# Kernel optimization log

Hardware: AMD Instinct MI355X
Metric: run time of the kernel (lower is better)

The kernel has to match this reference:

```python
import jax, jax.numpy as jnp
import numpy as np
import math

SIZE = (60, 270, 480)           # full video T, H, W
CHANNELS = 14                   # sum of per-level grid channels 8+4+2
GRID_SIZES = [(60, 16, 16, 8), (30, 8, 8, 4), (15, 4, 4, 2)]
IDX_MAX = (60, 3, 5)            # patch grid -> patch_size (1, 90, 96)
PADDING = (0, 1, 1)
N_PATCH = 64
MANIP_LBASE = 2.0
MANIP_LEVELS = 8
INIT_SCALE = 1e-3


def setup_inputs() -> dict:
    key = jax.random.key(0)
    kt, kh, kw = jax.random.split(key, 3)
    idx = jnp.stack([
        jax.random.randint(kt, (N_PATCH,), 0, IDX_MAX[0]),
        jax.random.randint(kh, (N_PATCH,), 0, IDX_MAX[1]),
        jax.random.randint(kw, (N_PATCH,), 0, IDX_MAX[2]),
    ], axis=1).astype(jnp.int32)
    inp = {
        "idx": idx,
        "idx_max": jnp.asarray(IDX_MAX, dtype=jnp.int32),
        "padding": jnp.asarray(PADDING, dtype=jnp.int32),
    }
    for i, (T, H, W, C) in enumerate(GRID_SIZES):
        k = jax.random.fold_in(key, 10 + i)
        inp[f"grid{i}"] = jax.random.normal(k, (T * H * W, C), jnp.float32) * INIT_SCALE
    return inp


def _pixel_idx_1d(ix, size_d, nmax_d, pad_d):
    # ix: [N] patch index along one dim -> ([N, P+2*pad] clipped pixel idx, mask)
    p = size_d // nmax_d
    offs = jnp.arange(-pad_d, p + pad_d)
    raw = ix[:, None] * p + offs[None, :]
    mask = ((raw >= 0) & (raw < size_d)).astype(jnp.float32)
    return jnp.clip(raw, 0, size_d - 1), mask


def reference(idx, idx_max, padding, grid0, grid1, grid2):
    T, H, W = SIZE
    im = tuple(int(v) for v in np.asarray(idx_max))
    pad = tuple(int(v) for v in np.asarray(padding))
    patch = tuple(SIZE[d] // im[d] for d in range(3))
    ppad = tuple(patch[d] + 2 * pad[d] for d in range(3))

    # Multi-level grids -> trilinear upsample to full (T,H,W,C_i), concat on C.
    # jax.image.resize 'trilinear' uses half-pixel centers == torch align_corners=False.
    enc_splits = []
    for g, (Tg, Hg, Wg, Cg) in zip((grid0, grid1, grid2), GRID_SIZES):
        enc_splits.append(jax.image.resize(g.reshape(Tg, Hg, Wg, Cg), (T, H, W, Cg), method="trilinear"))
    enc = jnp.concatenate(enc_splits, axis=-1).reshape(T * H * W, CHANNELS)

    it, mt = _pixel_idx_1d(idx[:, 0], T, im[0], pad[0])
    ih, mh = _pixel_idx_1d(idx[:, 1], H, im[1], pad[1])
    iw, mw = _pixel_idx_1d(idx[:, 2], W, im[2], pad[2])

    flat = (it[:, :, None, None] * (H * W) + ih[:, None, :, None] * W + iw[:, None, None, :]).reshape(-1)
    mask = (mt[:, :, None, None] * mh[:, None, :, None] * mw[:, None, None, :]).reshape(-1, 1)

    t_embed = (mask * enc[flat]).reshape((idx.shape[0],) + ppad + (CHANNELS,))

    bases = (MANIP_LBASE ** jnp.arange(MANIP_LEVELS, dtype=jnp.float32)) * math.pi
    v = idx[:, 0].astype(jnp.float32)[:, None] * bases
    t_manip = jnp.concatenate([jnp.sin(v), jnp.cos(v)], axis=-1)  # [N, 2*levels]

    return t_embed, t_manip
```

## Files before the change

### kernel.cpp

```cpp
#include <hip/hip_runtime.h>
#include <math.h>


#define N_PATCH 64
#define PPAD_H 92
#define PPAD_W 98
#define CH 14
#define ROWS_PER_BLOCK 4
#define BLOCKS_PER_PATCH 23
#define ELEMS_PER_ROW (PPAD_W * CH)
#define ELEMS_PER_PATCH (PPAD_H * ELEMS_PER_ROW)
#define TOTAL_EMBED (N_PATCH * ELEMS_PER_PATCH)
#define TOTAL_MANIP (N_PATCH * 16)

#define RB_STRIDE 72
#define L1_OFF 48
#define L2_OFF 64
#define V_ENTRIES (ROWS_PER_BLOCK * 70)

__device__ __forceinline__ float lerpf(float a, float b, float f) {
    return a + f * (b - a);
}

__device__ __forceinline__ int wcell0(int rw0, float sw, int Wg) {
    float x = ((float)rw0 + 0.5f) * sw - 0.5f;
    int w0 = (int)floorf(x);
    return min(max(w0, 0), Wg - 1);
}

__global__ __launch_bounds__(256) void embed_kernel(
    const int* __restrict__ idx,
    const float* __restrict__ g0,
    const float* __restrict__ g1,
    const float* __restrict__ g2,
    float* __restrict__ out)
{
    __shared__ __align__(16) float s_V[ROWS_PER_BLOCK * RB_STRIDE];
    __shared__ float4 s_wl[3][PPAD_W];
    __shared__ __align__(16) float s_buf[4 * 64 * CH];

    const int tid = threadIdx.x;
    const int bx  = blockIdx.x;
    const int n   = blockIdx.y;
    const int it  = idx[3 * n + 0];
    const int ih  = idx[3 * n + 1];
    const int iw  = idx[3 * n + 2];
    const int rw0 = iw * 96 - 1;
    const int row0 = bx * ROWS_PER_BLOCK;

    const float sw0 = (float)((double)16 / 480.0);
    const float sw1 = (float)((double)8  / 480.0);
    const float sw2 = (float)((double)4  / 480.0);
    const float sh0 = (float)((double)16 / 270.0);
    const float sh1 = (float)((double)8  / 270.0);
    const float sh2 = (float)((double)4  / 270.0);

    if (bx == 0 && n == 0) {
        float* om = out + TOTAL_EMBED;
        for (int e = tid; e < TOTAL_MANIP; e += 256) {
            int nn = e >> 4;
            int j  = e & 15;
            int l  = j & 7;
            float base = (float)M_PI * (float)(1 << l);
            float v = (float)idx[3 * nn + 0] * base;
            double dv = (double)v;
            om[e] = (float)((j < 8) ? sin(dv) : cos(dv));
        }
    }

    const int C0_0 = wcell0(rw0, sw0, 16);
    const int C0_1 = wcell0(rw0, sw1, 8);
    const int C0_2 = wcell0(rw0, sw2, 4);
    for (int e = tid; e < V_ENTRIES; e += 256) {
        int row = e / 70;
        int off = e - 70 * row;
        int rh  = ih * 90 + row0 + row - 1;
        float mh = ((unsigned)rh < 270u) ? 1.0f : 0.0f;
        float v;
        if (off < L1_OFF) {
            int cell = off >> 3, chn = off & 7;
            float xh = ((float)rh + 0.5f) * sh0 - 0.5f;
            float ff = floorf(xh);
            float fh = xh - ff;
            int h0 = (int)ff;
            int h0c = min(max(h0, 0), 15), h1c = min(h0 + 1, 15);
            int cw = min(C0_0 + cell, 15);
            const float* base = g0 + (size_t)it * 2048;
            float a = base[(h0c * 16 + cw) * 8 + chn];
            float b = base[(h1c * 16 + cw) * 8 + chn];
            v = mh * lerpf(a, b, fh);
        } else if (off < L2_OFF) {
            int o = off - L1_OFF;
            int cell = o >> 2, chn = o & 3;
            float xh = ((float)rh + 0.5f) * sh1 - 0.5f;
            float ff = floorf(xh);
            float fh = xh - ff;
            int h0 = (int)ff;
            int h0c = min(max(h0, 0), 7), h1c = min(h0 + 1, 7);
            float xt = ((float)it + 0.5f) * 0.5f - 0.5f;
            float ftf = floorf(xt);
            float ft  = xt - ftf;
            int t0 = (int)ftf;
            int t0c = min(max(t0, 0), 29), t1c = min(t0 + 1, 29);
            int cw = min(C0_1 + cell, 7);
            float a00 = g1[((t0c * 8 + h0c) * 8 + cw) * 4 + chn];
            float a01 = g1[((t0c * 8 + h1c) * 8 + cw) * 4 + chn];
            float a10 = g1[((t1c * 8 + h0c) * 8 + cw) * 4 + chn];
            float a11 = g1[((t1c * 8 + h1c) * 8 + cw) * 4 + chn];
            v = mh * lerpf(lerpf(a00, a01, fh), lerpf(a10, a11, fh), ft);
        } else {
            int o = off - L2_OFF;
            int cell = o >> 1, chn = o & 1;
            float xh = ((float)rh + 0.5f) * sh2 - 0.5f;
            float ff = floorf(xh);
            float fh = xh - ff;
            int h0 = (int)ff;
            int h0c = min(max(h0, 0), 3), h1c = min(h0 + 1, 3);
            float xt = ((float)it + 0.5f) * 0.25f - 0.5f;
            float ftf = floorf(xt);
            float ft  = xt - ftf;
            int t0 = (int)ftf;
            int t0c = min(max(t0, 0), 14), t1c = min(t0 + 1, 14);
            int cw = min(C0_2 + cell, 3);
            float a00 = g2[((t0c * 4 + h0c) * 4 + cw) * 2 + chn];
            float a01 = g2[((t0c * 4 + h1c) * 4 + cw) * 2 + chn];
            float a10 = g2[((t1c * 4 + h0c) * 4 + cw) * 2 + chn];
            float a11 = g2[((t1c * 4 + h1c) * 4 + cw) * 2 + chn];
            v = mh * lerpf(lerpf(a00, a01, fh), lerpf(a10, a11, fh), ft);
        }
        s_V[row * RB_STRIDE + off] = v;
    }

    for (int i = tid; i < 3 * PPAD_W; i += 256) {
        int lvl = (i >= PPAD_W) + (i >= 2 * PPAD_W);
        int ww  = i - PPAD_W * lvl;
        int Wg  = (lvl == 0) ? 16 : ((lvl == 1) ? 8 : 4);
        int cs  = (lvl == 0) ? 8  : ((lvl == 1) ? 4 : 2);
        int bb  = (lvl == 0) ? 0  : ((lvl == 1) ? L1_OFF : L2_OFF);
        int C0  = (lvl == 0) ? C0_0 : ((lvl == 1) ? C0_1 : C0_2);
        float sw = (lvl == 0) ? sw0 : ((lvl == 1) ? sw1 : sw2);
        int rw = iw * 96 + ww - 1;
        float mask = ((unsigned)rw < 480u) ? 1.0f : 0.0f;
        float x  = ((float)rw + 0.5f) * sw - 0.5f;
        float ff = floorf(x);
        float f  = x - ff;
        int w0 = (int)ff;
        int wa = min(max(w0, 0), Wg - 1);
        int wb = min(w0 + 1, Wg - 1);
        s_wl[lvl][ww] = make_float4(__int_as_float(bb + (wa - C0) * cs),
                                    __int_as_float(bb + (wb - C0) * cs), f, mask);
    }

    __syncthreads();

    const int wv   = tid >> 6;
    const int lane = tid & 63;
    float* lbuf = s_buf + wv * (64 * CH);
    const float* V = s_V + wv * RB_STRIDE;
    float* orow = out + (size_t)n * ELEMS_PER_PATCH
                      + (size_t)(row0 + wv) * ELEMS_PER_ROW;

    #pragma unroll
    for (int s = 0; s < 2; ++s) {
        asm volatile("s_waitcnt lgkmcnt(0)" ::: "memory");
        __builtin_amdgcn_sched_barrier(0);
        int ww = s * 64 + lane;
        if (ww < PPAD_W) {
            float4 wl0 = s_wl[0][ww];
            float4 wl1 = s_wl[1][ww];
            float4 wl2 = s_wl[2][ww];
            int oA0 = __float_as_int(wl0.x), oB0 = __float_as_int(wl0.y);
            int oA1 = __float_as_int(wl1.x), oB1 = __float_as_int(wl1.y);
            int oA2 = __float_as_int(wl2.x), oB2 = __float_as_int(wl2.y);
            float fw0 = wl0.z, fw1 = wl1.z, fw2 = wl2.z, mw = wl0.w;

            float4 A0  = *(const float4*)(V + oA0);
            float4 A1  = *(const float4*)(V + oA0 + 4);
            float4 B0  = *(const float4*)(V + oB0);
            float4 B1  = *(const float4*)(V + oB0 + 4);
            float4 C1a = *(const float4*)(V + oA1);
            float4 C1b = *(const float4*)(V + oB1);
            float2 C2a = *(const float2*)(V + oA2);
            float2 C2b = *(const float2*)(V + oB2);

            float2* b = (float2*)(lbuf + lane * CH);
            b[0] = make_float2(mw * lerpf(A0.x, B0.x, fw0),
                               mw * lerpf(A0.y, B0.y, fw0));
            b[1] = make_float2(mw * lerpf(A0.z, B0.z, fw0),
                               mw * lerpf(A0.w, B0.w, fw0));
            b[2] = make_float2(mw * lerpf(A1.x, B1.x, fw0),
                               mw * lerpf(A1.y, B1.y, fw0));
            b[3] = make_float2(mw * lerpf(A1.z, B1.z, fw0),
                               mw * lerpf(A1.w, B1.w, fw0));
            b[4] = make_float2(mw * lerpf(C1a.x, C1b.x, fw1),
                               mw * lerpf(C1a.y, C1b.y, fw1));
            b[5] = make_float2(mw * lerpf(C1a.z, C1b.z, fw1),
                               mw * lerpf(C1a.w, C1b.w, fw1));
            b[6] = make_float2(mw * lerpf(C2a.x, C2b.x, fw2),
                               mw * lerpf(C2a.y, C2b.y, fw2));
        }
        __builtin_amdgcn_wave_barrier();
        asm volatile("s_waitcnt lgkmcnt(0)" ::: "memory");
        __builtin_amdgcn_sched_barrier(0);

        const int npx = (s == 0) ? 64 : (PPAD_W - 64);
        const int nf4 = npx * CH / 4;
        const float4* sb = (const float4*)lbuf;
        float4* gb = (float4*)(orow + s * 64 * CH);
        for (int j = lane; j < nf4; j += 64) gb[j] = sb[j];
        __builtin_amdgcn_wave_barrier();
    }
}

extern "C" void kernel_launch(void* const* d_in, const int* in_sizes, int n_in,
                              void* d_out, int out_size, void* d_ws, size_t ws_size,
                              hipStream_t stream) {
    const int*   idx = (const int*)  d_in[0];
    const float* g0  = (const float*)d_in[3];
    const float* g1  = (const float*)d_in[4];
    const float* g2  = (const float*)d_in[5];
    float* out = (float*)d_out;

    dim3 grid(BLOCKS_PER_PATCH, N_PATCH);
    embed_kernel<<<grid, 256, 0, stream>>>(idx, g0, g1, g2, out);
}
```

Baseline: 13.60 us.

## Split into table-precompute kernel and direct-store streaming kernel via workspace

Splits the fused kernel in two. The first kernel computes the per-row height/time-interpolated value table for all patches into a global workspace, plus the sin/cos manip output. The second kernel launches one block per output row, with each thread computing two channel pairs and writing one float4 straight to global memory, so there is no LDS staging. This removes the per-block shared-memory setup and the syncs, but adds a second launch and a round trip through global memory for the table.

```diff
diff --git a/kernel.cpp b/kernel.cpp
--- a/kernel.cpp
+++ b/kernel.cpp
@@ -6,17 +6,19 @@
 #define PPAD_H 92
 #define PPAD_W 98
 #define CH 14
-#define ROWS_PER_BLOCK 4
-#define BLOCKS_PER_PATCH 23
 #define ELEMS_PER_ROW (PPAD_W * CH)
+#define F4_PER_ROW (ELEMS_PER_ROW / 4)
 #define ELEMS_PER_PATCH (PPAD_H * ELEMS_PER_ROW)
+#define F4_PER_PATCH (ELEMS_PER_PATCH / 4)
 #define TOTAL_EMBED (N_PATCH * ELEMS_PER_PATCH)
 #define TOTAL_MANIP (N_PATCH * 16)
 
 #define RB_STRIDE 72
 #define L1_OFF 48
 #define L2_OFF 64
-#define V_ENTRIES (ROWS_PER_BLOCK * 70)
+#define ROWS_TOTAL (N_PATCH * PPAD_H)
+#define V_TOTAL (ROWS_TOTAL * 70)
+#define WS_PATCH (PPAD_H * RB_STRIDE)
 
 __device__ __forceinline__ float lerpf(float a, float b, float f) {
     return a + f * (b - a);
@@ -28,188 +30,163 @@
     return min(max(w0, 0), Wg - 1);
 }
 
-__global__ __launch_bounds__(256) void embed_kernel(
+#define SW0 ((float)((double)16 / 480.0))
+#define SW1 ((float)((double)8  / 480.0))
+#define SW2 ((float)((double)4  / 480.0))
+#define SH0 ((float)((double)16 / 270.0))
+#define SH1 ((float)((double)8  / 270.0))
+#define SH2 ((float)((double)4  / 270.0))
+
+__global__ __launch_bounds__(256) void vtab_kernel(
     const int* __restrict__ idx,
     const float* __restrict__ g0,
     const float* __restrict__ g1,
     const float* __restrict__ g2,
+    float* __restrict__ ws,
     float* __restrict__ out)
 {
-    __shared__ __align__(16) float s_V[ROWS_PER_BLOCK * RB_STRIDE];
-    __shared__ float4 s_wl[3][PPAD_W];
-    __shared__ __align__(16) float s_buf[4 * 64 * CH];
-
-    const int tid = threadIdx.x;
-    const int bx  = blockIdx.x;
-    const int n   = blockIdx.y;
-    const int it  = idx[3 * n + 0];
-    const int ih  = idx[3 * n + 1];
-    const int iw  = idx[3 * n + 2];
-    const int rw0 = iw * 96 - 1;
-    const int row0 = bx * ROWS_PER_BLOCK;
-
-    const float sw0 = (float)((double)16 / 480.0);
-    const float sw1 = (float)((double)8  / 480.0);
-    const float sw2 = (float)((double)4  / 480.0);
-    const float sh0 = (float)((double)16 / 270.0);
-    const float sh1 = (float)((double)8  / 270.0);
-    const float sh2 = (float)((double)4  / 270.0);
-
-    if (bx == 0 && n == 0) {
-        float* om = out + TOTAL_EMBED;
-        for (int e = tid; e < TOTAL_MANIP; e += 256) {
+    int bx = blockIdx.x;
+    int tid = threadIdx.x;
+
+    if (bx >= 1610) {
+        int e = (bx - 1610) * 256 + tid;
+        if (e < TOTAL_MANIP) {
             int nn = e >> 4;
             int j  = e & 15;
             int l  = j & 7;
             float base = (float)M_PI * (float)(1 << l);
             float v = (float)idx[3 * nn + 0] * base;
             double dv = (double)v;
-            om[e] = (float)((j < 8) ? sin(dv) : cos(dv));
+            out[TOTAL_EMBED + e] = (float)((j < 8) ? sin(dv) : cos(dv));
         }
+        return;
     }
 
-    const int C0_0 = wcell0(rw0, sw0, 16);
-    const int C0_1 = wcell0(rw0, sw1, 8);
-    const int C0_2 = wcell0(rw0, sw2, 4);
-    for (int e = tid; e < V_ENTRIES; e += 256) {
-        int row = e / 70;
-        int off = e - 70 * row;
-        int rh  = ih * 90 + row0 + row - 1;
-        float mh = ((unsigned)rh < 270u) ? 1.0f : 0.0f;
-        float v;
-        if (off < L1_OFF) {
-            int cell = off >> 3, chn = off & 7;
-            float xh = ((float)rh + 0.5f) * sh0 - 0.5f;
-            float ff = floorf(xh);
-            float fh = xh - ff;
-            int h0 = (int)ff;
-            int h0c = min(max(h0, 0), 15), h1c = min(h0 + 1, 15);
-            int cw = min(C0_0 + cell, 15);
-            const float* base = g0 + (size_t)it * 2048;
-            float a = base[(h0c * 16 + cw) * 8 + chn];
-            float b = base[(h1c * 16 + cw) * 8 + chn];
-            v = mh * lerpf(a, b, fh);
-        } else if (off < L2_OFF) {
-            int o = off - L1_OFF;
-            int cell = o >> 2, chn = o & 3;
-            float xh = ((float)rh + 0.5f) * sh1 - 0.5f;
-            float ff = floorf(xh);
-            float fh = xh - ff;
-            int h0 = (int)ff;
-            int h0c = min(max(h0, 0), 7), h1c = min(h0 + 1, 7);
-            float xt = ((float)it + 0.5f) * 0.5f - 0.5f;
-            float ftf = floorf(xt);
-            float ft  = xt - ftf;
-            int t0 = (int)ftf;
-            int t0c = min(max(t0, 0), 29), t1c = min(t0 + 1, 29);
-            int cw = min(C0_1 + cell, 7);
-            float a00 = g1[((t0c * 8 + h0c) * 8 + cw) * 4 + chn];
-            float a01 = g1[((t0c * 8 + h1c) * 8 + cw) * 4 + chn];
-            float a10 = g1[((t1c * 8 + h0c) * 8 + cw) * 4 + chn];
-            float a11 = g1[((t1c * 8 + h1c) * 8 + cw) * 4 + chn];
-            v = mh * lerpf(lerpf(a00, a01, fh), lerpf(a10, a11, fh), ft);
-        } else {
-            int o = off - L2_OFF;
-            int cell = o >> 1, chn = o & 1;
-            float xh = ((float)rh + 0.5f) * sh2 - 0.5f;
-            float ff = floorf(xh);
-            float fh = xh - ff;
-            int h0 = (int)ff;
-            int h0c = min(max(h0, 0), 3), h1c = min(h0 + 1, 3);
-            float xt = ((float)it + 0.5f) * 0.25f - 0.5f;
-            float ftf = floorf(xt);
-            float ft  = xt - ftf;
-            int t0 = (int)ftf;
-            int t0c = min(max(t0, 0), 14), t1c = min(t0 + 1, 14);
-            int cw = min(C0_2 + cell, 3);
-            float a00 = g2[((t0c * 4 + h0c) * 4 + cw) * 2 + chn];
-            float a01 = g2[((t0c * 4 + h1c) * 4 + cw) * 2 + chn];
-            float a10 = g2[((t1c * 4 + h0c) * 4 + cw) * 2 + chn];
-            float a11 = g2[((t1c * 4 + h1c) * 4 + cw) * 2 + chn];
-            v = mh * lerpf(lerpf(a00, a01, fh), lerpf(a10, a11, fh), ft);
-        }
-        s_V[row * RB_STRIDE + off] = v;
+    int T = bx * 256 + tid;
+    int n   = T / (PPAD_H * 70);
+    int rem = T - n * (PPAD_H * 70);
+    int row = rem / 70;
+    int off = rem - row * 70;
+
+    int it = idx[3 * n + 0];
+    int ih = idx[3 * n + 1];
+    int iw = idx[3 * n + 2];
+    int rw0 = iw * 96 - 1;
+    int rh  = ih * 90 + row - 1;
+    float mh = ((unsigned)rh < 270u) ? 1.0f : 0.0f;
+    float v;
+
+    if (off < L1_OFF) {
+        int C0 = wcell0(rw0, SW0, 16);
+        int cell = off >> 3, chn = off & 7;
+        float xh = ((float)rh + 0.5f) * SH0 - 0.5f;
+        float ff = floorf(xh);
+        float fh = xh - ff;
+        int h0 = (int)ff;
+        int h0c = min(max(h0, 0), 15), h1c = min(h0 + 1, 15);
+        int cw = min(C0 + cell, 15);
+        const float* base = g0 + (size_t)it * 2048;
+        float a = base[(h0c * 16 + cw) * 8 + chn];
+        float b = base[(h1c * 16 + cw) * 8 + chn];
+        v = mh * lerpf(a, b, fh);
+    } else if (off < L2_OFF) {
+        int C0 = wcell0(rw0, SW1, 8);
+        int o = off - L1_OFF;
+        int cell = o >> 2, chn = o & 3;
+        float xh = ((float)rh + 0.5f) * SH1 - 0.5f;
+        float ff = floorf(xh);
+        float fh = xh - ff;
+        int h0 = (int)ff;
+        int h0c = min(max(h0, 0), 7), h1c = min(h0 + 1, 7);
+        float xt = ((float)it + 0.5f) * 0.5f - 0.5f;
+        float ftf = floorf(xt);
+        float ft  = xt - ftf;
+        int t0 = (int)ftf;
+        int t0c = min(max(t0, 0), 29), t1c = min(t0 + 1, 29);
+        int cw = min(C0 + cell, 7);
+        float a00 = g1[((t0c * 8 + h0c) * 8 + cw) * 4 + chn];
+        float a01 = g1[((t0c * 8 + h1c) * 8 + cw) * 4 + chn];
+        float a10 = g1[((t1c * 8 + h0c) * 8 + cw) * 4 + chn];
+        float a11 = g1[((t1c * 8 + h1c) * 8 + cw) * 4 + chn];
+        v = mh * lerpf(lerpf(a00, a01, fh), lerpf(a10, a11, fh), ft);
+    } else {
+        int C0 = wcell0(rw0, SW2, 4);
+        int o = off - L2_OFF;
+        int cell = o >> 1, chn = o & 1;
+        float xh = ((float)rh + 0.5f) * SH2 - 0.5f;
+        float ff = floorf(xh);
+        float fh = xh - ff;
+        int h0 = (int)ff;
+        int h0c = min(max(h0, 0), 3), h1c = min(h0 + 1, 3);
+        float xt = ((float)it + 0.5f) * 0.25f - 0.5f;
+        float ftf = floorf(xt);
+        float ft  = xt - ftf;
+        int t0 = (int)ftf;
+        int t0c = min(max(t0, 0), 14), t1c = min(t0 + 1, 14);
+        int cw = min(C0 + cell, 3);
+        float a00 = g2[((t0c * 4 + h0c) * 4 + cw) * 2 + chn];
+        float a01 = g2[((t0c * 4 + h1c) * 4 + cw) * 2 + chn];
+        float a10 = g2[((t1c * 4 + h0c) * 4 + cw) * 2 + chn];
+        float a11 = g2[((t1c * 4 + h1c) * 4 + cw) * 2 + chn];
+        v = mh * lerpf(lerpf(a00, a01, fh), lerpf(a10, a11, fh), ft);
     }
-
-    for (int i = tid; i < 3 * PPAD_W; i += 256) {
-        int lvl = (i >= PPAD_W) + (i >= 2 * PPAD_W);
-        int ww  = i - PPAD_W * lvl;
-        int Wg  = (lvl == 0) ? 16 : ((lvl == 1) ? 8 : 4);
-        int cs  = (lvl == 0) ? 8  : ((lvl == 1) ? 4 : 2);
-        int bb  = (lvl == 0) ? 0  : ((lvl == 1) ? L1_OFF : L2_OFF);
-        int C0  = (lvl == 0) ? C0_0 : ((lvl == 1) ? C0_1 : C0_2);
-        float sw = (lvl == 0) ? sw0 : ((lvl == 1) ? sw1 : sw2);
-        int rw = iw * 96 + ww - 1;
-        float mask = ((unsigned)rw < 480u) ? 1.0f : 0.0f;
-        float x  = ((float)rw + 0.5f) * sw - 0.5f;
-        float ff = floorf(x);
-        float f  = x - ff;
-        int w0 = (int)ff;
-        int wa = min(max(w0, 0), Wg - 1);
-        int wb = min(w0 + 1, Wg - 1);
-        s_wl[lvl][ww] = make_float4(__int_as_float(bb + (wa - C0) * cs),
-                                    __int_as_float(bb + (wb - C0) * cs), f, mask);
-    }
-
-    __syncthreads();
-
-    const int wv   = tid >> 6;
-    const int lane = tid & 63;
-    float* lbuf = s_buf + wv * (64 * CH);
-    const float* V = s_V + wv * RB_STRIDE;
-    float* orow = out + (size_t)n * ELEMS_PER_PATCH
-                      + (size_t)(row0 + wv) * ELEMS_PER_ROW;
-
-    #pragma unroll
-    for (int s = 0; s < 2; ++s) {
-        asm volatile("s_waitcnt lgkmcnt(0)" ::: "memory");
-        __builtin_amdgcn_sched_barrier(0);
-        int ww = s * 64 + lane;
-        if (ww < PPAD_W) {
-            float4 wl0 = s_wl[0][ww];
-            float4 wl1 = s_wl[1][ww];
-            float4 wl2 = s_wl[2][ww];
-            int oA0 = __float_as_int(wl0.x), oB0 = __float_as_int(wl0.y);
-            int oA1 = __float_as_int(wl1.x), oB1 = __float_as_int(wl1.y);
-            int oA2 = __float_as_int(wl2.x), oB2 = __float_as_int(wl2.y);
-            float fw0 = wl0.z, fw1 = wl1.z, fw2 = wl2.z, mw = wl0.w;
-
-            float4 A0  = *(const float4*)(V + oA0);
-            float4 A1  = *(const float4*)(V + oA0 + 4);
-            float4 B0  = *(const float4*)(V + oB0);
-            float4 B1  = *(const float4*)(V + oB0 + 4);
-            float4 C1a = *(const float4*)(V + oA1);
-            float4 C1b = *(const float4*)(V + oB1);
-            float2 C2a = *(const float2*)(V + oA2);
-            float2 C2b = *(const float2*)(V + oB2);
-
-            float2* b = (float2*)(lbuf + lane * CH);
-            b[0] = make_float2(mw * lerpf(A0.x, B0.x, fw0),
-                               mw * lerpf(A0.y, B0.y, fw0));
-            b[1] = make_float2(mw * lerpf(A0.z, B0.z, fw0),
-                               mw * lerpf(A0.w, B0.w, fw0));
-            b[2] = make_float2(mw * lerpf(A1.x, B1.x, fw0),
-                               mw * lerpf(A1.y, B1.y, fw0));
-            b[3] = make_float2(mw * lerpf(A1.z, B1.z, fw0),
-                               mw * lerpf(A1.w, B1.w, fw0));
-            b[4] = make_float2(mw * lerpf(C1a.x, C1b.x, fw1),
-                               mw * lerpf(C1a.y, C1b.y, fw1));
-            b[5] = make_float2(mw * lerpf(C1a.z, C1b.z, fw1),
-                               mw * lerpf(C1a.w, C1b.w, fw1));
-            b[6] = make_float2(mw * lerpf(C2a.x, C2b.x, fw2),
-                               mw * lerpf(C2a.y, C2b.y, fw2));
-        }
-        __builtin_amdgcn_wave_barrier();
-        asm volatile("s_waitcnt lgkmcnt(0)" ::: "memory");
-        __builtin_amdgcn_sched_barrier(0);
-
-        const int npx = (s == 0) ? 64 : (PPAD_W - 64);
-        const int nf4 = npx * CH / 4;
-        const float4* sb = (const float4*)lbuf;
-        float4* gb = (float4*)(orow + s * 64 * CH);
-        for (int j = lane; j < nf4; j += 64) gb[j] = sb[j];
-        __builtin_amdgcn_wave_barrier();
-    }
+    ws[n * WS_PATCH + row * RB_STRIDE + off] = v;
+}
+
+__device__ __forceinline__ void do_pair(int P, int iw, int C0_0, int C0_1, int C0_2,
+                                        const float* __restrict__ V,
+                                        float& rx, float& ry)
+{
+    int q = P % 7;
+    int p = P / 7;
+    int rw = iw * 96 + p - 1;
+    float mw = ((unsigned)rw < 480u) ? 1.0f : 0.0f;
+    int lvl = (q >= 4) + (q >= 6);
+
+    float sw = (lvl == 0) ? SW0 : ((lvl == 1) ? SW1 : SW2);
+    int Wg1  = (16 >> lvl) - 1;
+    int cs   = 8 >> lvl;
+    int bb   = (lvl == 0) ? 0 : ((lvl == 1) ? L1_OFF : L2_OFF);
+    int ch   = 2 * q - ((lvl == 0) ? 0 : ((lvl == 1) ? 8 : 12));
+    int C0   = (lvl == 0) ? C0_0 : ((lvl == 1) ? C0_1 : C0_2);
+
+    float x = ((float)rw + 0.5f) * sw - 0.5f;
+    float ffl = floorf(x);
+    float fw = x - ffl;
+    int w0 = (int)ffl;
+    int wa = min(max(w0, 0), Wg1);
+    int wb = min(w0 + 1, Wg1);
+    int oA = bb + (wa - C0) * cs + ch;
+    int oB = bb + (wb - C0) * cs + ch;
+    float2 A = *(const float2*)(V + oA);
+    float2 B = *(const float2*)(V + oB);
+    rx = mw * lerpf(A.x, B.x, fw);
+    ry = mw * lerpf(A.y, B.y, fw);
+}
+
+__global__ __launch_bounds__(384) void stream_kernel(
+    const int* __restrict__ idx,
+    const float* __restrict__ ws,
+    float* __restrict__ out)
+{
+    const int row = blockIdx.x;
+    const int n   = blockIdx.y;
+    const int j   = threadIdx.x;
+    if (j >= F4_PER_ROW) return;
+
+    const int iw = idx[3 * n + 2];
+    const int rw0 = iw * 96 - 1;
+    const int C0_0 = wcell0(rw0, SW0, 16);
+    const int C0_1 = wcell0(rw0, SW1, 8);
+    const int C0_2 = wcell0(rw0, SW2, 4);
+    const float* V = ws + n * WS_PATCH + row * RB_STRIDE;
+
+    float r0x, r0y, r1x, r1y;
+    do_pair(2 * j,     iw, C0_0, C0_1, C0_2, V, r0x, r0y);
+    do_pair(2 * j + 1, iw, C0_0, C0_1, C0_2, V, r1x, r1y);
+
+    float4* gb = (float4*)out + (size_t)n * F4_PER_PATCH + row * F4_PER_ROW + j;
+    *gb = make_float4(r0x, r0y, r1x, r1y);
 }
 
 extern "C" void kernel_launch(void* const* d_in, const int* in_sizes, int n_in,
@@ -220,7 +197,9 @@
     const float* g1  = (const float*)d_in[4];
     const float* g2  = (const float*)d_in[5];
     float* out = (float*)d_out;
-
-    dim3 grid(BLOCKS_PER_PATCH, N_PATCH);
-    embed_kernel<<<grid, 256, 0, stream>>>(idx, g0, g1, g2, out);
-}
+    float* ws  = (float*)d_ws;
+
+    vtab_kernel<<<1614, 256, 0, stream>>>(idx, g0, g1, g2, ws, out);
+    dim3 gridB(PPAD_H, N_PATCH);
+    stream_kernel<<<gridB, 384, 0, stream>>>(idx, ws, out);
+}
```

Result: slower. 20.80 us (+53.0%).
